# Optimization experiments

Hardware: AMD Instinct MI355X
Metric: run time of the kernel (lower is better)

## Reference

```python
import jax, jax.numpy as jnp
import numpy as np

N_T, N_I = 4096, 4096
TEXT_DIM, IMAGE_DIM, HIDDEN_DIM = 1024, 1024, 1024


def setup_inputs() -> dict:
    key = jax.random.key(0)
    ks = jax.random.split(key, 8)
    s_t = 1.0 / np.sqrt(TEXT_DIM)
    s_i = 1.0 / np.sqrt(IMAGE_DIM)
    return {
        "text_features": jax.random.normal(ks[0], (N_T, TEXT_DIM), jnp.float32),
        "image_features": jax.random.normal(ks[1], (N_I, IMAGE_DIM), jnp.float32),
        # nn.Linear params: weight [out, in], bias [out]
        "w_text": jax.random.uniform(ks[2], (HIDDEN_DIM, TEXT_DIM), jnp.float32, -s_t, s_t),
        "b_text": jax.random.uniform(ks[3], (HIDDEN_DIM,), jnp.float32, -s_t, s_t),
        "w_image": jax.random.uniform(ks[4], (HIDDEN_DIM, IMAGE_DIM), jnp.float32, -s_i, s_i),
        "b_image": jax.random.uniform(ks[5], (HIDDEN_DIM,), jnp.float32, -s_i, s_i),
        "scale_TI": jnp.ones((1,), jnp.float32),
        "scale_IT": jnp.ones((1,), jnp.float32),
    }


def reference(text_features, image_features, w_text, b_text, w_image, b_image, scale_TI, scale_IT):
    # linear projections to shared hidden space
    t = text_features @ w_text.T + b_text      # [N_t, H]
    i = image_features @ w_image.T + b_image   # [N_i, H]
    inv_sqrt_h = 1.0 / jnp.sqrt(jnp.asarray(HIDDEN_DIM, t.dtype))
    # text -> image attention: softmax over image axis, scaled post-softmax
    logits_TI = (t @ i.T) * inv_sqrt_h               # [N_t, N_i]
    attn_TI = jax.nn.softmax(logits_TI, axis=-1) * scale_TI
    # image -> text attention
    attn_IT = jax.nn.softmax(logits_TI.T, axis=-1) * scale_IT  # [N_i, N_t]
    text_attention_on_image = attn_TI @ image_features  # [N_t, image_dim]
    image_attention_on_text = attn_IT @ text_features   # [N_i, text_dim]
    return (text_attention_on_image, image_attention_on_text)
```

## Files before the change

kernel.cpp:

```cpp
#include <hip/hip_runtime.h>


typedef __bf16 bf16x8 __attribute__((ext_vector_type(8)));
typedef float f32x4 __attribute__((ext_vector_type(4)));

#define N_T 4096
#define N_I 4096
#define DIM 1024
#define TSS 136

__device__ __forceinline__ unsigned short f2bf(float f) {
    unsigned int u = __float_as_uint(f);
    u += 0x7fffu + ((u >> 16) & 1u);
    return (unsigned short)(u >> 16);
}

__device__ __forceinline__ void async_cp16(const unsigned short* g, unsigned short* l) {
    __builtin_amdgcn_global_load_lds(
        (const __attribute__((address_space(1))) unsigned int*)g,
        (__attribute__((address_space(3))) unsigned int*)l, 16, 0, 0);
}

__device__ __forceinline__ void stage_async(const unsigned short* __restrict__ src,
                                            int ld, int row0, int k0,
                                            unsigned short* lds, int t) {
    int r = t >> 2, c = (t & 3) << 3;
    const unsigned short* g = src + (size_t)(row0 + r) * ld + k0 + c;
    async_cp16(g, lds + r * 32 + c);
    async_cp16(g + (size_t)64 * ld, lds + (64 + r) * 32 + c);
}

__device__ __forceinline__ void mfma_step(const unsigned short* As,
                                          const unsigned short* Bs, f32x4 acc[4][4],
                                          int wrow, int wcol, int lane16, int quad) {
    bf16x8 a[4], b[4];
#pragma unroll
    for (int i = 0; i < 4; ++i) {
        a[i] = *(const bf16x8*)&As[(wrow + i * 16 + lane16) * 32 + quad * 8];
        b[i] = *(const bf16x8*)&Bs[(wcol + i * 16 + lane16) * 32 + quad * 8];
    }
#pragma unroll
    for (int i = 0; i < 4; ++i)
#pragma unroll
        for (int j = 0; j < 4; ++j)
            acc[i][j] = __builtin_amdgcn_mfma_f32_16x16x32_bf16(a[i], b[j], acc[i][j], 0, 0, 0);
}

__device__ __forceinline__ void tile_store(const unsigned short* sm,
                                           unsigned short* __restrict__ g, int ld,
                                           int row0, int col0, int tid) {
    int r = tid >> 1, h = (tid & 1) << 6;
    const unsigned short* src = sm + r * TSS + h;
    unsigned short* dst = g + (size_t)(row0 + r) * ld + col0 + h;
#pragma unroll
    for (int v = 0; v < 8; ++v)
        *(uint4*)(dst + v * 8) = *(const uint4*)(src + v * 8);
}

#define GEMM_IDX()                                               \
    int tid = threadIdx.x;                                       \
    int m0 = blockIdx.x * 128, n0 = blockIdx.y * 128;            \
    int lane = tid & 63, wave = tid >> 6;                        \
    int lane16 = lane & 15, quad = lane >> 4;                    \
    int wrow = (wave >> 1) * 64, wcol = (wave & 1) * 64;         \
    f32x4 acc[4][4];                                             \
    {                                                            \
        f32x4 z = {0.f, 0.f, 0.f, 0.f};                          \
        for (int i = 0; i < 4; ++i)                              \
            for (int j = 0; j < 4; ++j) acc[i][j] = z;           \
    }

__global__ void __launch_bounds__(256)
cvt_w(const float* __restrict__ wt, const float* __restrict__ wi,
      unsigned short* __restrict__ wtb, unsigned short* __restrict__ wib) {
    size_t i = (size_t)(blockIdx.x * 256 + threadIdx.x) * 8;
    const float* s;
    unsigned short* d;
    size_t off;
    if (i < 1048576) { s = wt; d = wtb; off = i; }
    else             { s = wi; d = wib; off = i - 1048576; }
    float4 f0 = *(const float4*)(s + off);
    float4 f1 = *(const float4*)(s + off + 4);
    uint4 o;
    o.x = (unsigned int)f2bf(f0.x) | ((unsigned int)f2bf(f0.y) << 16);
    o.y = (unsigned int)f2bf(f0.z) | ((unsigned int)f2bf(f0.w) << 16);
    o.z = (unsigned int)f2bf(f1.x) | ((unsigned int)f2bf(f1.y) << 16);
    o.w = (unsigned int)f2bf(f1.z) | ((unsigned int)f2bf(f1.w) << 16);
    *(uint4*)(d + off) = o;
}

__global__ void __launch_bounds__(256)
cvt_tr_fused(const float* __restrict__ im, const float* __restrict__ tx,
             unsigned short* __restrict__ imb, unsigned short* __restrict__ txb,
             unsigned short* __restrict__ imgT, unsigned short* __restrict__ textT) {
    const float* in = blockIdx.z ? tx : im;
    unsigned short* nb = blockIdx.z ? txb : imb;
    unsigned short* tr = blockIdx.z ? textT : imgT;
    __shared__ float tile[32][33];
    int c0 = blockIdx.x * 32, r0 = blockIdx.y * 32;
    int txi = threadIdx.x & 31, tyi = threadIdx.x >> 5;
#pragma unroll
    for (int i = tyi; i < 32; i += 8) {
        float v = in[(size_t)(r0 + i) * DIM + c0 + txi];
        tile[i][txi] = v;
        nb[(size_t)(r0 + i) * DIM + c0 + txi] = f2bf(v);
    }
    __syncthreads();
#pragma unroll
    for (int i = tyi; i < 32; i += 8)
        tr[(size_t)(c0 + i) * N_T + r0 + txi] = f2bf(tile[txi][i]);
}

__global__ void __launch_bounds__(256, 4)
gemm_proj2(const unsigned short* __restrict__ Atx, const unsigned short* __restrict__ Wtx,
           const float* __restrict__ btx, unsigned short* __restrict__ Ctx,
           const unsigned short* __restrict__ Aim, const unsigned short* __restrict__ Wim,
           const float* __restrict__ bim, unsigned short* __restrict__ Cim) {
    __shared__ unsigned short As[2][128 * 32];
    __shared__ unsigned short Bs[2][128 * 32];
    int z = blockIdx.z;
    const unsigned short* A = z ? Aim : Atx;
    const unsigned short* W = z ? Wim : Wtx;
    const float* bias = z ? bim : btx;
    unsigned short* C = z ? Cim : Ctx;
    GEMM_IDX();
    for (int k0 = 0; k0 < DIM; k0 += 64) {
        stage_async(A, DIM, m0, k0, As[0], tid);
        stage_async(W, DIM, n0, k0, Bs[0], tid);
        stage_async(A, DIM, m0, k0 + 32, As[1], tid);
        stage_async(W, DIM, n0, k0 + 32, Bs[1], tid);
        __syncthreads();
        mfma_step(As[0], Bs[0], acc, wrow, wcol, lane16, quad);
        mfma_step(As[1], Bs[1], acc, wrow, wcol, lane16, quad);
        __syncthreads();
    }
#pragma unroll
    for (int j = 0; j < 4; ++j) {
        int col = n0 + wcol + j * 16 + lane16;
        float bv = bias[col];
#pragma unroll
        for (int i = 0; i < 4; ++i) {
            int rowb = m0 + wrow + i * 16 + quad * 4;
#pragma unroll
            for (int r = 0; r < 4; ++r)
                C[(size_t)(rowb + r) * DIM + col] = f2bf(acc[i][j][r] + bv);
        }
    }
}

__global__ void __launch_bounds__(256, 4)
gemm_logits_exp(const unsigned short* __restrict__ Tb,
                const unsigned short* __restrict__ Ib,
                unsigned short* __restrict__ P, unsigned short* __restrict__ PT,
                float* __restrict__ lT, float* __restrict__ lI) {
    __shared__ unsigned short smem[128 * TSS];
    unsigned short* As0 = smem;
    unsigned short* Bs0 = smem + 4096;
    unsigned short* As1 = smem + 8192;
    unsigned short* Bs1 = smem + 12288;
    GEMM_IDX();
    for (int k0 = 0; k0 < DIM; k0 += 64) {
        stage_async(Tb, DIM, m0, k0, As0, tid);
        stage_async(Ib, DIM, n0, k0, Bs0, tid);
        stage_async(Tb, DIM, m0, k0 + 32, As1, tid);
        stage_async(Ib, DIM, n0, k0 + 32, Bs1, tid);
        __syncthreads();
        mfma_step(As0, Bs0, acc, wrow, wcol, lane16, quad);
        mfma_step(As1, Bs1, acc, wrow, wcol, lane16, quad);
        __syncthreads();
    }
#pragma unroll
    for (int i = 0; i < 4; ++i)
#pragma unroll
        for (int j = 0; j < 4; ++j)
#pragma unroll
            for (int r = 0; r < 4; ++r)
                acc[i][j][r] = __expf(acc[i][j][r] * 0.03125f);
#pragma unroll
    for (int i = 0; i < 4; ++i)
#pragma unroll
        for (int r = 0; r < 4; ++r) {
            float s = acc[i][0][r] + acc[i][1][r] + acc[i][2][r] + acc[i][3][r];
            s += __shfl_xor(s, 1); s += __shfl_xor(s, 2);
            s += __shfl_xor(s, 4); s += __shfl_xor(s, 8);
            if (lane16 == 0) atomicAdd(&lT[m0 + wrow + i * 16 + quad * 4 + r], s);
        }
#pragma unroll
    for (int j = 0; j < 4; ++j) {
        float s = 0.f;
#pragma unroll
        for (int i = 0; i < 4; ++i)
#pragma unroll
            for (int r = 0; r < 4; ++r) s += acc[i][j][r];
        s += __shfl_xor(s, 16); s += __shfl_xor(s, 32);
        if (quad == 0) atomicAdd(&lI[n0 + wcol + j * 16 + lane16], s);
    }
    __syncthreads();
#pragma unroll
    for (int i = 0; i < 4; ++i)
#pragma unroll
        for (int j = 0; j < 4; ++j)
#pragma unroll
            for (int r = 0; r < 4; ++r)
                smem[(wrow + i * 16 + quad * 4 + r) * TSS + wcol + j * 16 + lane16] =
                    f2bf(acc[i][j][r]);
    __syncthreads();
    tile_store(smem, P, N_I, m0, n0, tid);
    __syncthreads();
#pragma unroll
    for (int i = 0; i < 4; ++i)
#pragma unroll
        for (int j = 0; j < 4; ++j) {
            unsigned int lo = (unsigned int)f2bf(acc[i][j][0]) |
                              ((unsigned int)f2bf(acc[i][j][1]) << 16);
            unsigned int hi = (unsigned int)f2bf(acc[i][j][2]) |
                              ((unsigned int)f2bf(acc[i][j][3]) << 16);
            uint2 v; v.x = lo; v.y = hi;
            *(uint2*)&smem[(wcol + j * 16 + lane16) * TSS + wrow + i * 16 + quad * 4] = v;
        }
    __syncthreads();
    tile_store(smem, PT, N_T, n0, m0, tid);
}

__global__ void __launch_bounds__(512, 4)
gemm_attn2(const unsigned short* __restrict__ P, const unsigned short* __restrict__ imgT,
           const float* __restrict__ lT, const float* __restrict__ sTI,
           float* __restrict__ out0,
           const unsigned short* __restrict__ PT, const unsigned short* __restrict__ textT,
           const float* __restrict__ lI, const float* __restrict__ sIT,
           float* __restrict__ out1) {
    __shared__ unsigned short As[2][2][128 * 32];
    __shared__ unsigned short Bs[2][2][128 * 32];
    int which = blockIdx.z;
    const unsigned short* A = which ? PT : P;
    const unsigned short* Bt = which ? textT : imgT;
    const float* l = which ? lI : lT;
    const float* sp = which ? sIT : sTI;
    float* out = which ? out1 : out0;

    int tid = threadIdx.x;
    int half = tid >> 8;
    int t = tid & 255;
    int m0 = blockIdx.x * 128, n0 = blockIdx.y * 128;
    int lane = tid & 63;
    int wv = (tid >> 6) & 3;
    int lane16 = lane & 15, quad = lane >> 4;
    int wrow = (wv >> 1) * 64, wcol = (wv & 1) * 64;
    f32x4 acc[4][4];
    {
        f32x4 z = {0.f, 0.f, 0.f, 0.f};
        for (int i = 0; i < 4; ++i)
            for (int j = 0; j < 4; ++j) acc[i][j] = z;
    }

    int kbeg = half * 2048;
    for (int k0 = kbeg; k0 < kbeg + 2048; k0 += 64) {
        stage_async(A, 4096, m0, k0, As[half][0], t);
        stage_async(Bt, 4096, n0, k0, Bs[half][0], t);
        stage_async(A, 4096, m0, k0 + 32, As[half][1], t);
        stage_async(Bt, 4096, n0, k0 + 32, Bs[half][1], t);
        __syncthreads();
        mfma_step(As[half][0], Bs[half][0], acc, wrow, wcol, lane16, quad);
        mfma_step(As[half][1], Bs[half][1], acc, wrow, wcol, lane16, quad);
        __syncthreads();
    }

    float* red = (float*)As;
#pragma unroll
    for (int i = 0; i < 4; ++i) {
        __syncthreads();
        if (half) {
#pragma unroll
            for (int j = 0; j < 4; ++j)
                *(f32x4*)&red[wv * 1024 + lane * 16 + j * 4] = acc[i][j];
        }
        __syncthreads();
        if (!half) {
#pragma unroll
            for (int j = 0; j < 4; ++j)
                acc[i][j] += *(const f32x4*)&red[wv * 1024 + lane * 16 + j * 4];
        }
    }
    if (half) return;

    float sc = sp[0];
#pragma unroll
    for (int i = 0; i < 4; ++i) {
        int rowb = m0 + wrow + i * 16 + quad * 4;
        float fac[4];
#pragma unroll
        for (int r = 0; r < 4; ++r) fac[r] = sc / l[rowb + r];
#pragma unroll
        for (int j = 0; j < 4; ++j) {
            int col = n0 + wcol + j * 16 + lane16;
#pragma unroll
            for (int r = 0; r < 4; ++r)
                out[(size_t)(rowb + r) * DIM + col] = acc[i][j][r] * fac[r];
        }
    }
}

extern "C" void kernel_launch(void* const* d_in, const int* in_sizes, int n_in,
                              void* d_out, int out_size, void* d_ws, size_t ws_size,
                              hipStream_t stream) {
    const float* text = (const float*)d_in[0];
    const float* image = (const float*)d_in[1];
    const float* w_text = (const float*)d_in[2];
    const float* b_text = (const float*)d_in[3];
    const float* w_image = (const float*)d_in[4];
    const float* b_image = (const float*)d_in[5];
    const float* scale_TI = (const float*)d_in[6];
    const float* scale_IT = (const float*)d_in[7];
    float* out0 = (float*)d_out;
    float* out1 = out0 + (size_t)N_T * DIM;

    char* ws = (char*)d_ws;
    unsigned short* text_bf = (unsigned short*)(ws);
    unsigned short* image_bf = (unsigned short*)(ws + (8ull << 20));
    unsigned short* wt_bf = (unsigned short*)(ws + (16ull << 20));
    unsigned short* wi_bf = (unsigned short*)(ws + (18ull << 20));
    unsigned short* P = (unsigned short*)(ws);
    unsigned short* imgT = (unsigned short*)(ws + (32ull << 20));
    unsigned short* textT = (unsigned short*)(ws + (40ull << 20));
    unsigned short* t_bf = (unsigned short*)(ws + (48ull << 20));
    unsigned short* i_bf = (unsigned short*)(ws + (56ull << 20));
    unsigned short* PT = (unsigned short*)(ws + (64ull << 20));
    float* lT = (float*)(ws + (96ull << 20));
    float* lI = (float*)(ws + (96ull << 20) + 16384);

    hipMemsetAsync(lT, 0, 32768, stream);

    cvt_w<<<1024, 256, 0, stream>>>(w_text, w_image, wt_bf, wi_bf);
    cvt_tr_fused<<<dim3(DIM / 32, N_T / 32, 2), 256, 0, stream>>>(
        image, text, image_bf, text_bf, imgT, textT);

    gemm_proj2<<<dim3(N_T / 128, DIM / 128, 2), 256, 0, stream>>>(
        text_bf, wt_bf, b_text, t_bf, image_bf, wi_bf, b_image, i_bf);

    gemm_logits_exp<<<dim3(N_T / 128, N_I / 128), 256, 0, stream>>>(t_bf, i_bf, P, PT, lT, lI);

    gemm_attn2<<<dim3(N_T / 128, DIM / 128, 2), 512, 0, stream>>>(
        P, imgT, lT, scale_TI, out0, PT, textT, lI, scale_IT, out1);
}
```

Measured before the change: 270.8 us.

## Split-K the projection GEMM across two wave groups and fold memset into cvt_w

The projection GEMM now runs 512-thread blocks in which two halves each handle half of the K dimension. Their accumulators are then merged through LDS, as the attention GEMM already does. The hipMemsetAsync of the row-sum buffers is removed, and zeroing is moved into the first blocks of the weight-conversion kernel. The aim is more waves per tile to hide latency in a short-K GEMM and one fewer API call, at the cost of double the LDS and an added reduction step.

```diff
diff --git a/kernel.cpp b/kernel.cpp
--- a/kernel.cpp
+++ b/kernel.cpp
@@ -57,23 +57,51 @@
         *(uint4*)(dst + v * 8) = *(const uint4*)(src + v * 8);
 }
 
-#define GEMM_IDX()                                               \
-    int tid = threadIdx.x;                                       \
+#define SPLITK_IDX()                                             \
+    int tid = threadIdx.x;                           \
+    int half = tid >> 8;               \
+    int t = tid & 255;                                           \
     int m0 = blockIdx.x * 128, n0 = blockIdx.y * 128;            \
-    int lane = tid & 63, wave = tid >> 6;                        \
+    int lane = tid & 63;                                         \
+    int wv = (tid >> 6) & 3;                                     \
     int lane16 = lane & 15, quad = lane >> 4;                    \
-    int wrow = (wave >> 1) * 64, wcol = (wave & 1) * 64;         \
+    int wrow = (wv >> 1) * 64, wcol = (wv & 1) * 64;             \
     f32x4 acc[4][4];                                             \
     {                                                            \
-        f32x4 z = {0.f, 0.f, 0.f, 0.f};                          \
+        f32x4 z = {0.f, 0.f, 0.f, 0.f};                         \
         for (int i = 0; i < 4; ++i)                              \
             for (int j = 0; j < 4; ++j) acc[i][j] = z;           \
     }
 
+#define SPLITK_MERGE(AsBase)                                     \
+    {                                                            \
+        float* red = (float*)(AsBase);                           \
+        _Pragma("unroll")                                        \
+        for (int i = 0; i < 4; ++i) {                            \
+            __syncthreads();                                     \
+            if (half) {                                          \
+                _Pragma("unroll")                                \
+                for (int j = 0; j < 4; ++j)                      \
+                    *(f32x4*)&red[wv * 1024 + lane * 16 + j * 4] = acc[i][j]; \
+            }                                                    \
+            __syncthreads();                                     \
+            if (!half) {                                         \
+                _Pragma("unroll")                                \
+                for (int j = 0; j < 4; ++j)                      \
+                    acc[i][j] += *(const f32x4*)&red[wv * 1024 + lane * 16 + j * 4]; \
+            }                                                    \
+        }                                                        \
+    }
+
 __global__ void __launch_bounds__(256)
 cvt_w(const float* __restrict__ wt, const float* __restrict__ wi,
-      unsigned short* __restrict__ wtb, unsigned short* __restrict__ wib) {
+      unsigned short* __restrict__ wtb, unsigned short* __restrict__ wib,
+      float* __restrict__ lTI) {
     size_t i = (size_t)(blockIdx.x * 256 + threadIdx.x) * 8;
+    if (blockIdx.x < 4) {
+        *(f32x4*)&lTI[(blockIdx.x * 256 + threadIdx.x) * 8] = (f32x4){0.f, 0.f, 0.f, 0.f};
+        *(f32x4*)&lTI[(blockIdx.x * 256 + threadIdx.x) * 8 + 4] = (f32x4){0.f, 0.f, 0.f, 0.f};
+    }
     const float* s;
     unsigned short* d;
     size_t off;
@@ -111,29 +139,32 @@
         tr[(size_t)(c0 + i) * N_T + r0 + txi] = f2bf(tile[txi][i]);
 }
 
-__global__ void __launch_bounds__(256, 4)
+__global__ void __launch_bounds__(512, 4)
 gemm_proj2(const unsigned short* __restrict__ Atx, const unsigned short* __restrict__ Wtx,
            const float* __restrict__ btx, unsigned short* __restrict__ Ctx,
            const unsigned short* __restrict__ Aim, const unsigned short* __restrict__ Wim,
            const float* __restrict__ bim, unsigned short* __restrict__ Cim) {
-    __shared__ unsigned short As[2][128 * 32];
-    __shared__ unsigned short Bs[2][128 * 32];
+    __shared__ unsigned short As[2][2][128 * 32];
+    __shared__ unsigned short Bs[2][2][128 * 32];
     int z = blockIdx.z;
     const unsigned short* A = z ? Aim : Atx;
     const unsigned short* W = z ? Wim : Wtx;
     const float* bias = z ? bim : btx;
     unsigned short* C = z ? Cim : Ctx;
-    GEMM_IDX();
-    for (int k0 = 0; k0 < DIM; k0 += 64) {
-        stage_async(A, DIM, m0, k0, As[0], tid);
-        stage_async(W, DIM, n0, k0, Bs[0], tid);
-        stage_async(A, DIM, m0, k0 + 32, As[1], tid);
-        stage_async(W, DIM, n0, k0 + 32, Bs[1], tid);
-        __syncthreads();
-        mfma_step(As[0], Bs[0], acc, wrow, wcol, lane16, quad);
-        mfma_step(As[1], Bs[1], acc, wrow, wcol, lane16, quad);
-        __syncthreads();
-    }
+    SPLITK_IDX();
+    int kbeg = half * 512;
+    for (int k0 = kbeg; k0 < kbeg + 512; k0 += 64) {
+        stage_async(A, DIM, m0, k0, As[half][0], t);
+        stage_async(W, DIM, n0, k0, Bs[half][0], t);
+        stage_async(A, DIM, m0, k0 + 32, As[half][1], t);
+        stage_async(W, DIM, n0, k0 + 32, Bs[half][1], t);
+        __syncthreads();
+        mfma_step(As[half][0], Bs[half][0], acc, wrow, wcol, lane16, quad);
+        mfma_step(As[half][1], Bs[half][1], acc, wrow, wcol, lane16, quad);
+        __syncthreads();
+    }
+    SPLITK_MERGE(As);
+    if (half) return;
 #pragma unroll
     for (int j = 0; j < 4; ++j) {
         int col = n0 + wcol + j * 16 + lane16;
@@ -158,7 +189,17 @@
     unsigned short* Bs0 = smem + 4096;
     unsigned short* As1 = smem + 8192;
     unsigned short* Bs1 = smem + 12288;
-    GEMM_IDX();
+    int tid = threadIdx.x;
+    int m0 = blockIdx.x * 128, n0 = blockIdx.y * 128;
+    int lane = tid & 63, wave = tid >> 6;
+    int lane16 = lane & 15, quad = lane >> 4;
+    int wrow = (wave >> 1) * 64, wcol = (wave & 1) * 64;
+    f32x4 acc[4][4];
+    {
+        f32x4 z = {0.f, 0.f, 0.f, 0.f};
+        for (int i = 0; i < 4; ++i)
+            for (int j = 0; j < 4; ++j) acc[i][j] = z;
+    }
     for (int k0 = 0; k0 < DIM; k0 += 64) {
         stage_async(Tb, DIM, m0, k0, As0, tid);
         stage_async(Ib, DIM, n0, k0, Bs0, tid);
@@ -237,22 +278,7 @@
     const float* l = which ? lI : lT;
     const float* sp = which ? sIT : sTI;
     float* out = which ? out1 : out0;
-
-    int tid = threadIdx.x;
-    int half = tid >> 8;
-    int t = tid & 255;
-    int m0 = blockIdx.x * 128, n0 = blockIdx.y * 128;
-    int lane = tid & 63;
-    int wv = (tid >> 6) & 3;
-    int lane16 = lane & 15, quad = lane >> 4;
-    int wrow = (wv >> 1) * 64, wcol = (wv & 1) * 64;
-    f32x4 acc[4][4];
-    {
-        f32x4 z = {0.f, 0.f, 0.f, 0.f};
-        for (int i = 0; i < 4; ++i)
-            for (int j = 0; j < 4; ++j) acc[i][j] = z;
-    }
-
+    SPLITK_IDX();
     int kbeg = half * 2048;
     for (int k0 = kbeg; k0 < kbeg + 2048; k0 += 64) {
         stage_async(A, 4096, m0, k0, As[half][0], t);
@@ -264,25 +290,8 @@
         mfma_step(As[half][1], Bs[half][1], acc, wrow, wcol, lane16, quad);
         __syncthreads();
     }
-
-    float* red = (float*)As;
-#pragma unroll
-    for (int i = 0; i < 4; ++i) {
-        __syncthreads();
-        if (half) {
-#pragma unroll
-            for (int j = 0; j < 4; ++j)
-                *(f32x4*)&red[wv * 1024 + lane * 16 + j * 4] = acc[i][j];
-        }
-        __syncthreads();
-        if (!half) {
-#pragma unroll
-            for (int j = 0; j < 4; ++j)
-                acc[i][j] += *(const f32x4*)&red[wv * 1024 + lane * 16 + j * 4];
-        }
-    }
+    SPLITK_MERGE(As);
     if (half) return;
-
     float sc = sp[0];
 #pragma unroll
     for (int i = 0; i < 4; ++i) {
@@ -328,13 +337,11 @@
     float* lT = (float*)(ws + (96ull << 20));
     float* lI = (float*)(ws + (96ull << 20) + 16384);
 
-    hipMemsetAsync(lT, 0, 32768, stream);
-
-    cvt_w<<<1024, 256, 0, stream>>>(w_text, w_image, wt_bf, wi_bf);
+    cvt_w<<<1024, 256, 0, stream>>>(w_text, w_image, wt_bf, wi_bf, lT);
     cvt_tr_fused<<<dim3(DIM / 32, N_T / 32, 2), 256, 0, stream>>>(
         image, text, image_bf, text_bf, imgT, textT);
 
-    gemm_proj2<<<dim3(N_T / 128, DIM / 128, 2), 256, 0, stream>>>(
+    gemm_proj2<<<dim3(N_T / 128, DIM / 128, 2), 512, 0, stream>>>(
         text_bf, wt_bf, b_text, t_bf, image_bf, wi_bf, b_image, i_bf);
 
     gemm_logits_exp<<<dim3(N_T / 128, N_I / 128), 256, 0, stream>>>(t_bf, i_bf, P, PT, lT, lI);
```

Result: no change. 272.8 us (+0.8%).

## Fuse weight conversion, input transpose and memset into one prep kernel

Applied to the files above, without the earlier changes.

Merges the memset of the softmax-denominator buffers, the weight fp32-to-bf16 conversion and the input convert+transpose into a single launch, using the z grid dimension to select the job. The transpose tile grows to 64x64 and uses float4 loads and 16-byte bf16 stores instead of scalar element accesses. This removes two launches and improves memory vectorization in the prep phase. The transposed read from the padded LDS tile with stride 65 may introduce bank conflicts.

```diff
diff --git a/kernel.cpp b/kernel.cpp
--- a/kernel.cpp
+++ b/kernel.cpp
@@ -57,58 +57,75 @@
         *(uint4*)(dst + v * 8) = *(const uint4*)(src + v * 8);
 }
 
-#define GEMM_IDX()                                               \
-    int tid = threadIdx.x;                                       \
-    int m0 = blockIdx.x * 128, n0 = blockIdx.y * 128;            \
-    int lane = tid & 63, wave = tid >> 6;                        \
-    int lane16 = lane & 15, quad = lane >> 4;                    \
-    int wrow = (wave >> 1) * 64, wcol = (wave & 1) * 64;         \
-    f32x4 acc[4][4];                                             \
-    {                                                            \
-        f32x4 z = {0.f, 0.f, 0.f, 0.f};                          \
-        for (int i = 0; i < 4; ++i)                              \
-            for (int j = 0; j < 4; ++j) acc[i][j] = z;           \
-    }
-
 __global__ void __launch_bounds__(256)
-cvt_w(const float* __restrict__ wt, const float* __restrict__ wi,
-      unsigned short* __restrict__ wtb, unsigned short* __restrict__ wib) {
-    size_t i = (size_t)(blockIdx.x * 256 + threadIdx.x) * 8;
-    const float* s;
-    unsigned short* d;
-    size_t off;
-    if (i < 1048576) { s = wt; d = wtb; off = i; }
-    else             { s = wi; d = wib; off = i - 1048576; }
-    float4 f0 = *(const float4*)(s + off);
-    float4 f1 = *(const float4*)(s + off + 4);
-    uint4 o;
-    o.x = (unsigned int)f2bf(f0.x) | ((unsigned int)f2bf(f0.y) << 16);
-    o.y = (unsigned int)f2bf(f0.z) | ((unsigned int)f2bf(f0.w) << 16);
-    o.z = (unsigned int)f2bf(f1.x) | ((unsigned int)f2bf(f1.y) << 16);
-    o.w = (unsigned int)f2bf(f1.z) | ((unsigned int)f2bf(f1.w) << 16);
-    *(uint4*)(d + off) = o;
-}
-
-__global__ void __launch_bounds__(256)
-cvt_tr_fused(const float* __restrict__ im, const float* __restrict__ tx,
-             unsigned short* __restrict__ imb, unsigned short* __restrict__ txb,
-             unsigned short* __restrict__ imgT, unsigned short* __restrict__ textT) {
+cvt_all(const float* __restrict__ im, const float* __restrict__ tx,
+        const float* __restrict__ wt, const float* __restrict__ wi,
+        unsigned short* __restrict__ imb, unsigned short* __restrict__ txb,
+        unsigned short* __restrict__ imgT, unsigned short* __restrict__ textT,
+        unsigned short* __restrict__ wtb, unsigned short* __restrict__ wib,
+        float* __restrict__ lTI) {
+    int t = threadIdx.x;
+    if (blockIdx.z == 2) {
+        int lin = blockIdx.y * 64 + blockIdx.x;
+        if (lin < 4) {
+            *(f32x4*)&lTI[(lin * 256 + t) * 8] = (f32x4){0.f, 0.f, 0.f, 0.f};
+            *(f32x4*)&lTI[(lin * 256 + t) * 8 + 4] = (f32x4){0.f, 0.f, 0.f, 0.f};
+        }
+        size_t i = (size_t)(lin * 256 + t) * 8;
+        const float* s;
+        unsigned short* d;
+        size_t off;
+        if (i < 1048576) { s = wt; d = wtb; off = i; }
+        else             { s = wi; d = wib; off = i - 1048576; }
+        float4 f0 = *(const float4*)(s + off);
+        float4 f1 = *(const float4*)(s + off + 4);
+        uint4 o;
+        o.x = (unsigned int)f2bf(f0.x) | ((unsigned int)f2bf(f0.y) << 16);
+        o.y = (unsigned int)f2bf(f0.z) | ((unsigned int)f2bf(f0.w) << 16);
+        o.z = (unsigned int)f2bf(f1.x) | ((unsigned int)f2bf(f1.y) << 16);
+        o.w = (unsigned int)f2bf(f1.z) | ((unsigned int)f2bf(f1.w) << 16);
+        *(uint4*)(d + off) = o;
+        return;
+    }
     const float* in = blockIdx.z ? tx : im;
     unsigned short* nb = blockIdx.z ? txb : imb;
     unsigned short* tr = blockIdx.z ? textT : imgT;
-    __shared__ float tile[32][33];
-    int c0 = blockIdx.x * 32, r0 = blockIdx.y * 32;
-    int txi = threadIdx.x & 31, tyi = threadIdx.x >> 5;
-#pragma unroll
-    for (int i = tyi; i < 32; i += 8) {
-        float v = in[(size_t)(r0 + i) * DIM + c0 + txi];
-        tile[i][txi] = v;
-        nb[(size_t)(r0 + i) * DIM + c0 + txi] = f2bf(v);
-    }
-    __syncthreads();
-#pragma unroll
-    for (int i = tyi; i < 32; i += 8)
-        tr[(size_t)(c0 + i) * N_T + r0 + txi] = f2bf(tile[txi][i]);
+    __shared__ float tile[64][65];
+    int row0 = blockIdx.x * 64, col0 = blockIdx.y * 64;
+    int r = t >> 2, c = (t & 3) << 4;
+    {
+        const float* p = in + (size_t)(row0 + r) * DIM + col0 + c;
+        float4 f0 = *(const float4*)(p);
+        float4 f1 = *(const float4*)(p + 4);
+        float4 f2 = *(const float4*)(p + 8);
+        float4 f3 = *(const float4*)(p + 12);
+        *(float4*)&tile[r][c] = f0;
+        *(float4*)&tile[r][c + 4] = f1;
+        *(float4*)&tile[r][c + 8] = f2;
+        *(float4*)&tile[r][c + 12] = f3;
+        uint4 o0, o1;
+        o0.x = (unsigned int)f2bf(f0.x) | ((unsigned int)f2bf(f0.y) << 16);
+        o0.y = (unsigned int)f2bf(f0.z) | ((unsigned int)f2bf(f0.w) << 16);
+        o0.z = (unsigned int)f2bf(f1.x) | ((unsigned int)f2bf(f1.y) << 16);
+        o0.w = (unsigned int)f2bf(f1.z) | ((unsigned int)f2bf(f1.w) << 16);
+        o1.x = (unsigned int)f2bf(f2.x) | ((unsigned int)f2bf(f2.y) << 16);
+        o1.y = (unsigned int)f2bf(f2.z) | ((unsigned int)f2bf(f2.w) << 16);
+        o1.z = (unsigned int)f2bf(f3.x) | ((unsigned int)f2bf(f3.y) << 16);
+        o1.w = (unsigned int)f2bf(f3.z) | ((unsigned int)f2bf(f3.w) << 16);
+        unsigned short* q = nb + (size_t)(row0 + r) * DIM + col0 + c;
+        *(uint4*)q = o0;
+        *(uint4*)(q + 8) = o1;
+    }
+    __syncthreads();
+    {
+        int cr = r, cc = c;
+        unsigned short v[16];
+#pragma unroll
+        for (int u = 0; u < 16; ++u) v[u] = f2bf(tile[cc + u][cr]);
+        unsigned short* q = tr + (size_t)(col0 + cr) * N_T + row0 + cc;
+        *(uint4*)q = *(uint4*)&v[0];
+        *(uint4*)(q + 8) = *(uint4*)&v[8];
+    }
 }
 
 __global__ void __launch_bounds__(256, 4)
@@ -123,7 +140,17 @@
     const unsigned short* W = z ? Wim : Wtx;
     const float* bias = z ? bim : btx;
     unsigned short* C = z ? Cim : Ctx;
-    GEMM_IDX();
+    int tid = threadIdx.x;
+    int m0 = blockIdx.x * 128, n0 = blockIdx.y * 128;
+    int lane = tid & 63, wave = tid >> 6;
+    int lane16 = lane & 15, quad = lane >> 4;
+    int wrow = (wave >> 1) * 64, wcol = (wave & 1) * 64;
+    f32x4 acc[4][4];
+    {
+        f32x4 zz = {0.f, 0.f, 0.f, 0.f};
+        for (int i = 0; i < 4; ++i)
+            for (int j = 0; j < 4; ++j) acc[i][j] = zz;
+    }
     for (int k0 = 0; k0 < DIM; k0 += 64) {
         stage_async(A, DIM, m0, k0, As[0], tid);
         stage_async(W, DIM, n0, k0, Bs[0], tid);
@@ -158,7 +185,17 @@
     unsigned short* Bs0 = smem + 4096;
     unsigned short* As1 = smem + 8192;
     unsigned short* Bs1 = smem + 12288;
-    GEMM_IDX();
+    int tid = threadIdx.x;
+    int m0 = blockIdx.x * 128, n0 = blockIdx.y * 128;
+    int lane = tid & 63, wave = tid >> 6;
+    int lane16 = lane & 15, quad = lane >> 4;
+    int wrow = (wave >> 1) * 64, wcol = (wave & 1) * 64;
+    f32x4 acc[4][4];
+    {
+        f32x4 z = {0.f, 0.f, 0.f, 0.f};
+        for (int i = 0; i < 4; ++i)
+            for (int j = 0; j < 4; ++j) acc[i][j] = z;
+    }
     for (int k0 = 0; k0 < DIM; k0 += 64) {
         stage_async(Tb, DIM, m0, k0, As0, tid);
         stage_async(Ib, DIM, n0, k0, Bs0, tid);
@@ -328,11 +365,9 @@
     float* lT = (float*)(ws + (96ull << 20));
     float* lI = (float*)(ws + (96ull << 20) + 16384);
 
-    hipMemsetAsync(lT, 0, 32768, stream);
-
-    cvt_w<<<1024, 256, 0, stream>>>(w_text, w_image, wt_bf, wi_bf);
-    cvt_tr_fused<<<dim3(DIM / 32, N_T / 32, 2), 256, 0, stream>>>(
-        image, text, image_bf, text_bf, imgT, textT);
+    cvt_all<<<dim3(N_T / 64, DIM / 64, 3), 256, 0, stream>>>(
+        image, text, w_text, w_image, image_bf, text_bf, imgT, textT,
+        wt_bf, wi_bf, lT);
 
     gemm_proj2<<<dim3(N_T / 128, DIM / 128, 2), 256, 0, stream>>>(
         text_bf, wt_bf, b_text, t_bf, image_bf, wi_bf, b_image, i_bf);
```

Result: no change. 267.1 us (-1.3%).
